# Kernel tuning notes

Hardware: AMD Instinct MI355X
Metric: run time of the kernel (lower is better)

## Reference

```python
import jax, jax.numpy as jnp
import numpy as np

TEMP = 0.07
BASE_TEMP = 0.07
EPS = 1e-8


def setup_inputs() -> dict:
    key = jax.random.key(0)
    features = jax.random.normal(key, (4096, 2, 128), dtype=jnp.float32)
    return {"features": features}


def reference(features):
    B, V, D = features.shape  # bsz, n_views, dim
    # torch.cat(torch.unbind(features, dim=1), dim=0): view-major ordering
    cf = jnp.swapaxes(features, 0, 1).reshape(V * B, D)  # [N, D], N = V*B
    # cosine similarity = normalize rows then GEMM (same math as broadcasted CosineSimilarity)
    n = cf / jnp.maximum(jnp.linalg.norm(cf, axis=-1, keepdims=True), EPS)
    logits = jnp.matmul(n, n.T) / TEMP  # [N, N]
    N = V * B
    logits_mask = 1.0 - jnp.eye(N, dtype=logits.dtype)  # zero out self-contrast
    # SimCLR mask: eye(B) tiled over (anchor_count, contrast_count), minus diagonal
    pos_mask = jnp.tile(jnp.eye(B, dtype=logits.dtype), (V, V)) * logits_mask
    exp_logits = jnp.exp(logits) * logits_mask
    log_prob = logits - jnp.log(exp_logits.sum(axis=1, keepdims=True))
    mean_log_prob_pos = (pos_mask * log_prob).sum(axis=1) / pos_mask.sum(axis=1)
    loss = -(TEMP / BASE_TEMP) * mean_log_prob_pos
    return loss.reshape(V, B).mean()
```

## Files before the change

kernel.cpp:

```cpp
#include <hip/hip_runtime.h>
#include <hip/hip_bf16.h>
#include <math.h>


constexpr int   Bsz   = 4096;
constexpr int   Nrows = 8192;
constexpr int   Dd    = 128;
constexpr float TEMPf = 0.07f;
constexpr float EPSN  = 1e-8f;
constexpr float SCALE = 1.4426950408889634f / 0.07f;
constexpr float LN2   = 0.6931471805599453f;

constexpr int CHUNKS     = 16;
constexpr int CHUNK_COLS = Nrows / CHUNKS;
constexpr int TILE_COLS  = 64;
constexpr int TILES      = CHUNK_COLS / TILE_COLS;
constexpr int ROWS_BLK   = 128;
constexpr int PREPBLKS   = Bsz / 4;

typedef __attribute__((ext_vector_type(8)))  short bf16x8;
typedef __attribute__((ext_vector_type(16))) float floatx16;

constexpr size_t OFF_NA   = 0x200000;
constexpr size_t OFF_PART = 0x400000;
constexpr size_t OFF_SPOS = 0x480000;

__global__ void prep_k(const float* __restrict__ f,
                       __hip_bfloat16* __restrict__ nB,
                       __hip_bfloat16* __restrict__ nA,
                       float* __restrict__ sposPart,
                       float* __restrict__ out) {
    __shared__ float sred[4];
    int tid  = threadIdx.x;
    int wid  = tid >> 6;
    int lane = tid & 63;
    int b    = blockIdx.x * 4 + wid;
    if (blockIdx.x == 0 && tid == 0) out[0] = 0.f;

    const float* s0 = f + (size_t)(b * 2) * Dd;
    float2 x = *(const float2*)(s0 + lane * 2);
    float2 y = *(const float2*)(s0 + Dd + lane * 2);
    float ss0 = x.x * x.x + x.y * x.y;
    float ss1 = y.x * y.x + y.y * y.y;
    float dt  = x.x * y.x + x.y * y.y;
    #pragma unroll
    for (int off = 32; off; off >>= 1) {
        ss0 += __shfl_xor(ss0, off);
        ss1 += __shfl_xor(ss1, off);
        dt  += __shfl_xor(dt,  off);
    }
    float inv0 = 1.0f / fmaxf(sqrtf(ss0), EPSN);
    float inv1 = 1.0f / fmaxf(sqrtf(ss1), EPSN);
    __hip_bfloat162 h;
    h.x = __float2bfloat16(x.x * inv0);
    h.y = __float2bfloat16(x.y * inv0);
    *(__hip_bfloat162*)(nB + (size_t)b * Dd + lane * 2) = h;
    h.x = __float2bfloat16(x.x * inv0 * SCALE);
    h.y = __float2bfloat16(x.y * inv0 * SCALE);
    *(__hip_bfloat162*)(nA + (size_t)b * Dd + lane * 2) = h;
    h.x = __float2bfloat16(y.x * inv1);
    h.y = __float2bfloat16(y.y * inv1);
    *(__hip_bfloat162*)(nB + (size_t)(Bsz + b) * Dd + lane * 2) = h;
    h.x = __float2bfloat16(y.x * inv1 * SCALE);
    h.y = __float2bfloat16(y.y * inv1 * SCALE);
    *(__hip_bfloat162*)(nA + (size_t)(Bsz + b) * Dd + lane * 2) = h;

    if (lane == 0) sred[wid] = dt * inv0 * inv1 / TEMPf;
    __syncthreads();
    if (tid == 0) sposPart[blockIdx.x] = sred[0] + sred[1] + sred[2] + sred[3];
}

__global__ __launch_bounds__(256, 4)
void main_k(const __hip_bfloat16* __restrict__ nA, const __hip_bfloat16* __restrict__ nB,
            float* __restrict__ partial) {
    __shared__ char lds[TILE_COLS * 256];
    const int tid  = threadIdx.x;
    const int wid  = tid >> 6;
    const int lane = tid & 63;
    const int lo   = lane & 31;
    const int hi   = lane >> 5;
    const int rbase = blockIdx.y * ROWS_BLK + wid * 32;
    const int cbase = blockIdx.x * CHUNK_COLS;
    const char* gb  = (const char*)nB + (size_t)cbase * 256;
    const int su = tid & 15, scq = tid >> 4;

    bf16x8 afrag[8];
    {
        const char* rowp = (const char*)nA + (size_t)(rbase + lo) * 256 + hi * 16;
        #pragma unroll
        for (int kc = 0; kc < 8; kc++)
            afrag[kc] = *(const bf16x8*)(rowp + kc * 32);
    }

    float sums[16];
    #pragma unroll
    for (int r = 0; r < 16; r++) sums[r] = 0.f;

    floatx16 zero = {};

    #pragma unroll 1
    for (int t = 0; t < TILES; t++) {
        __syncthreads();
        {
            const char* g = gb + (size_t)t * (TILE_COLS * 256) + tid * 16;
            #pragma unroll
            for (int i = 0; i < 4; i++) {
                uint4 d = *(const uint4*)(g + i * 4096);
                int c = i * 16 + scq;
                *(uint4*)&lds[su * 1024 + ((c ^ su) & 63) * 16] = d;
            }
        }
        __syncthreads();

        floatx16 acc0 = zero, acc1 = zero;
        #pragma unroll
        for (int kc = 0; kc < 8; kc++) {
            int u = kc * 2 + hi;
            int a0 = u * 1024 + ((lo ^ u) & 63) * 16;
            bf16x8 b0 = *(const bf16x8*)&lds[a0];
            bf16x8 b1 = *(const bf16x8*)&lds[a0 ^ 512];
            acc0 = __builtin_amdgcn_mfma_f32_32x32x16_bf16(afrag[kc], b0, acc0, 0, 0, 0);
            acc1 = __builtin_amdgcn_mfma_f32_32x32x16_bf16(afrag[kc], b1, acc1, 0, 0, 0);
        }

        #pragma unroll
        for (int cg = 0; cg < 2; cg++) {
            const floatx16& acc = cg ? acc1 : acc0;
            bool dt_hit = (cbase + t * TILE_COLS + cg * 32 == rbase);
            #pragma unroll
            for (int r = 0; r < 16; r++) {
                float e = __builtin_amdgcn_exp2f(acc[r]);
                if (dt_hit && lo == ((r & 3) + 8 * (r >> 2) + 4 * hi)) e = 0.f;
                sums[r] += e;
            }
        }
    }

    #pragma unroll
    for (int r = 0; r < 16; r++) {
        float v = sums[r];
        #pragma unroll
        for (int off = 1; off < 32; off <<= 1) v += __shfl_xor(v, off);
        sums[r] = v;
    }
    if (lo == 0) {
        float* prow = partial + (size_t)blockIdx.x * Nrows;
        #pragma unroll
        for (int r = 0; r < 16; r++) {
            int grow = rbase + (r & 3) + 8 * (r >> 2) + 4 * hi;
            prow[grow] = sums[r];
        }
    }
}

__global__ __launch_bounds__(256)
void final_k(const float* __restrict__ partial, const float* __restrict__ sposPart,
             float* __restrict__ out) {
    __shared__ float red[4];
    int tid = threadIdx.x;
    int r = blockIdx.x * 256 + tid;
    float se = 0.f;
    #pragma unroll
    for (int p = 0; p < CHUNKS; p++) se += partial[(size_t)p * Nrows + r];
    float acc = __builtin_amdgcn_logf(se) * LN2;
    if (tid < 32) acc -= 2.f * sposPart[blockIdx.x * 32 + tid];
    #pragma unroll
    for (int off = 32; off; off >>= 1) acc += __shfl_xor(acc, off);
    if ((tid & 63) == 0) red[tid >> 6] = acc;
    __syncthreads();
    if (tid == 0)
        atomicAdd(out, (red[0] + red[1] + red[2] + red[3]) / (float)Nrows);
}

extern "C" void kernel_launch(void* const* d_in, const int* in_sizes, int n_in,
                              void* d_out, int out_size, void* d_ws, size_t ws_size,
                              hipStream_t stream) {
    const float* f = (const float*)d_in[0];
    char* ws = (char*)d_ws;
    __hip_bfloat16* nB = (__hip_bfloat16*)ws;
    __hip_bfloat16* nA = (__hip_bfloat16*)(ws + OFF_NA);
    float* partial     = (float*)(ws + OFF_PART);
    float* sposPart    = (float*)(ws + OFF_SPOS);

    prep_k<<<PREPBLKS, 256, 0, stream>>>(f, nB, nA, sposPart, (float*)d_out);
    dim3 grid(CHUNKS, Nrows / ROWS_BLK);
    main_k<<<grid, 256, 0, stream>>>(nA, nB, partial);
    final_k<<<Nrows / 256, 256, 0, stream>>>(partial, sposPart, (float*)d_out);
}
```

Measured before the change: 82.49 us.

## Drop LDS staging; load B fragments directly from global with 64-row warp tiles

The main kernel no longer stages column tiles of nB through shared memory with block barriers. Each warp now holds A fragments for 64 rows and reads B fragments straight from global/L2, reusing each B fragment across two MFMAs. The grid now uses 32 column chunks and 256-row blocks, with the partial buffer grown to match. This removes LDS traffic and __syncthreads but makes every warp issue redundant global loads of the same B data. It also doubles register use for accumulators and fragments, with launch bounds relaxed to 3.

```diff
diff --git a/kernel.cpp b/kernel.cpp
--- a/kernel.cpp
+++ b/kernel.cpp
@@ -11,11 +11,10 @@
 constexpr float SCALE = 1.4426950408889634f / 0.07f;
 constexpr float LN2   = 0.6931471805599453f;
 
-constexpr int CHUNKS     = 16;
+constexpr int CHUNKS     = 32;
 constexpr int CHUNK_COLS = Nrows / CHUNKS;
-constexpr int TILE_COLS  = 64;
-constexpr int TILES      = CHUNK_COLS / TILE_COLS;
-constexpr int ROWS_BLK   = 128;
+constexpr int CTS        = CHUNK_COLS / 32;
+constexpr int ROWS_BLK   = 256;
 constexpr int PREPBLKS   = Bsz / 4;
 
 typedef __attribute__((ext_vector_type(8)))  short bf16x8;
@@ -23,7 +22,7 @@
 
 constexpr size_t OFF_NA   = 0x200000;
 constexpr size_t OFF_PART = 0x400000;
-constexpr size_t OFF_SPOS = 0x480000;
+constexpr size_t OFF_SPOS = 0x500000;
 
 __global__ void prep_k(const float* __restrict__ f,
                        __hip_bfloat16* __restrict__ nB,
@@ -70,86 +69,78 @@
     if (tid == 0) sposPart[blockIdx.x] = sred[0] + sred[1] + sred[2] + sred[3];
 }
 
-__global__ __launch_bounds__(256, 4)
+__global__ __launch_bounds__(256, 3)
 void main_k(const __hip_bfloat16* __restrict__ nA, const __hip_bfloat16* __restrict__ nB,
             float* __restrict__ partial) {
-    __shared__ char lds[TILE_COLS * 256];
     const int tid  = threadIdx.x;
     const int wid  = tid >> 6;
     const int lane = tid & 63;
     const int lo   = lane & 31;
     const int hi   = lane >> 5;
-    const int rbase = blockIdx.y * ROWS_BLK + wid * 32;
+    const int rbase = blockIdx.y * ROWS_BLK + wid * 64;
     const int cbase = blockIdx.x * CHUNK_COLS;
-    const char* gb  = (const char*)nB + (size_t)cbase * 256;
-    const int su = tid & 15, scq = tid >> 4;
 
-    bf16x8 afrag[8];
-    {
-        const char* rowp = (const char*)nA + (size_t)(rbase + lo) * 256 + hi * 16;
+    bf16x8 afrag[2][8];
+    #pragma unroll
+    for (int s = 0; s < 2; s++) {
+        const char* rowp = (const char*)nA + (size_t)(rbase + s * 32 + lo) * 256 + hi * 16;
         #pragma unroll
         for (int kc = 0; kc < 8; kc++)
-            afrag[kc] = *(const bf16x8*)(rowp + kc * 32);
+            afrag[s][kc] = *(const bf16x8*)(rowp + kc * 32);
     }
 
-    float sums[16];
+    float sums[2][16];
     #pragma unroll
-    for (int r = 0; r < 16; r++) sums[r] = 0.f;
+    for (int s = 0; s < 2; s++)
+        #pragma unroll
+        for (int r = 0; r < 16; r++) sums[s][r] = 0.f;
 
     floatx16 zero = {};
+    const char* bp = (const char*)nB + (size_t)(cbase + lo) * 256 + hi * 16;
 
     #pragma unroll 1
-    for (int t = 0; t < TILES; t++) {
-        __syncthreads();
-        {
-            const char* g = gb + (size_t)t * (TILE_COLS * 256) + tid * 16;
-            #pragma unroll
-            for (int i = 0; i < 4; i++) {
-                uint4 d = *(const uint4*)(g + i * 4096);
-                int c = i * 16 + scq;
-                *(uint4*)&lds[su * 1024 + ((c ^ su) & 63) * 16] = d;
-            }
-        }
-        __syncthreads();
-
+    for (int ct = 0; ct < CTS; ct++) {
+        const char* bcol = bp + (size_t)ct * 32 * 256;
         floatx16 acc0 = zero, acc1 = zero;
         #pragma unroll
         for (int kc = 0; kc < 8; kc++) {
-            int u = kc * 2 + hi;
-            int a0 = u * 1024 + ((lo ^ u) & 63) * 16;
-            bf16x8 b0 = *(const bf16x8*)&lds[a0];
-            bf16x8 b1 = *(const bf16x8*)&lds[a0 ^ 512];
-            acc0 = __builtin_amdgcn_mfma_f32_32x32x16_bf16(afrag[kc], b0, acc0, 0, 0, 0);
-            acc1 = __builtin_amdgcn_mfma_f32_32x32x16_bf16(afrag[kc], b1, acc1, 0, 0, 0);
+            bf16x8 bf = *(const bf16x8*)(bcol + kc * 32);
+            acc0 = __builtin_amdgcn_mfma_f32_32x32x16_bf16(afrag[0][kc], bf, acc0, 0, 0, 0);
+            acc1 = __builtin_amdgcn_mfma_f32_32x32x16_bf16(afrag[1][kc], bf, acc1, 0, 0, 0);
         }
 
+        const int cb32 = cbase + ct * 32;
         #pragma unroll
-        for (int cg = 0; cg < 2; cg++) {
-            const floatx16& acc = cg ? acc1 : acc0;
-            bool dt_hit = (cbase + t * TILE_COLS + cg * 32 == rbase);
+        for (int s = 0; s < 2; s++) {
+            const floatx16& acc = s ? acc1 : acc0;
+            bool dt_hit = (cb32 == rbase + s * 32);
             #pragma unroll
             for (int r = 0; r < 16; r++) {
                 float e = __builtin_amdgcn_exp2f(acc[r]);
                 if (dt_hit && lo == ((r & 3) + 8 * (r >> 2) + 4 * hi)) e = 0.f;
-                sums[r] += e;
+                sums[s][r] += e;
             }
         }
     }
 
     #pragma unroll
-    for (int r = 0; r < 16; r++) {
-        float v = sums[r];
+    for (int s = 0; s < 2; s++)
         #pragma unroll
-        for (int off = 1; off < 32; off <<= 1) v += __shfl_xor(v, off);
-        sums[r] = v;
-    }
+        for (int r = 0; r < 16; r++) {
+            float v = sums[s][r];
+            #pragma unroll
+            for (int off = 1; off < 32; off <<= 1) v += __shfl_xor(v, off);
+            sums[s][r] = v;
+        }
     if (lo == 0) {
         float* prow = partial + (size_t)blockIdx.x * Nrows;
         #pragma unroll
-        for (int r = 0; r < 16; r++) {
-            int grow = rbase + (r & 3) + 8 * (r >> 2) + 4 * hi;
-            prow[grow] = sums[r];
-        }
+        for (int s = 0; s < 2; s++)
+            #pragma unroll
+            for (int r = 0; r < 16; r++) {
+                int grow = rbase + s * 32 + (r & 3) + 8 * (r >> 2) + 4 * hi;
+                prow[grow] = sums[s][r];
+            }
     }
 }
 
```

New measurement: 104.0 us. +26.1%, slower.
